# Optimization experiments

Hardware: AMD Instinct MI355X
Metric: run time of the kernel (lower is better)

## Reference

```python
import jax, jax.numpy as jnp
import numpy as np
from jax import lax

NUM_POINT = 2048   # S: number of FPS-sampled centers
RADIUS = 0.2       # ball-query radius
NUM_SAMPLE = 32    # K: neighbors per center


def setup_inputs() -> dict:
    key = jax.random.key(0)
    k1, k2 = jax.random.split(key)
    B, N, C = 4, 8192, 64
    xyz = jax.random.normal(k1, (B, N, 3), dtype=jnp.float32)
    features = jax.random.normal(k2, (B, C, N), dtype=jnp.float32)
    return {"xyz": xyz, "features": features}


def fps(xyz, npoint):
    """D-FPS (farthest point sampling on coords). xyz (B,N,3) -> idx (B,npoint) int32.
    Matches CUDA FPS: start at index 0, iteratively pick argmax of min-dist."""
    B, N, _ = xyz.shape

    def body(carry, _):
        min_d, last = carry
        p = jnp.take_along_axis(xyz, last[:, None, None], axis=1)  # (B,1,3)
        d = jnp.sum((xyz - p) ** 2, axis=-1)                        # (B,N)
        min_d = jnp.minimum(min_d, d)
        nxt = jnp.argmax(min_d, axis=-1).astype(jnp.int32)
        return (min_d, nxt), nxt

    idx0 = jnp.zeros((B,), jnp.int32)
    min_d0 = jnp.full((B, N), 1e10, dtype=xyz.dtype)
    (_, _), rest = lax.scan(body, (min_d0, idx0), None, length=npoint - 1)
    return jnp.concatenate([idx0[None], rest], axis=0).T  # (B, npoint)


def ball_query(radius, nsample, xyz, new_xyz):
    """For each center pick the first nsample point indices (in original order)
    with squared dist < radius^2; pad short lists with the first hit (0 if none).
    xyz (B,N,3), new_xyz (B,S,3) -> idx (B,S,nsample) int32."""
    N = xyz.shape[1]
    d2 = jnp.sum((new_xyz[:, :, None, :] - xyz[:, None, :, :]) ** 2, axis=-1)  # (B,S,N)
    mask = d2 < radius * radius
    # key = point index where in-ball, else N; nsample smallest keys = first hits in order
    key = jnp.where(mask, jnp.arange(N, dtype=jnp.int32)[None, None, :], N)
    _, idx = lax.top_k(-key, nsample)            # (B,S,nsample)
    idx = idx.astype(jnp.int32)
    valid = jnp.take_along_axis(mask, idx, axis=-1)
    first = jnp.where(valid[:, :, :1], idx[:, :, :1], 0)
    return jnp.where(valid, idx, first)


def reference(xyz, features):
    B, N, _ = xyz.shape
    C = features.shape[1]
    fps_idx = fps(xyz, NUM_POINT)                                       # (B,S)
    new_xyz = jnp.take_along_axis(xyz, fps_idx[:, :, None], axis=1)     # (B,S,3)
    idx = ball_query(RADIUS, NUM_SAMPLE, xyz, new_xyz)                  # (B,S,K)
    # grouped xyz, recentered on each sampled point
    grouped_xyz = jnp.take_along_axis(xyz[:, None], idx[..., None], axis=2)  # (B,S,K,3)
    grouped_xyz = grouped_xyz - new_xyz[:, :, None, :]
    # grouped features
    f = jnp.swapaxes(features, 1, 2)                                    # (B,N,C)
    grouped_f = jnp.take_along_axis(f[:, None], idx[..., None], axis=2)  # (B,S,K,C)
    # use_xyz=True: concat relative coords with features -> (B, 3+C, S, K)
    grouped = jnp.concatenate([grouped_xyz, grouped_f], axis=-1).transpose(0, 3, 1, 2)
    return (new_xyz, grouped, fps_idx)
```

## Files before the change

kernel.cpp:

```cpp
#include <hip/hip_runtime.h>

#define NPTS 8192
#define SPTS 2048
#define KS 32
#define CF 64
#define BQ 4
#define FPS_T 512
#define PPT (NPTS / FPS_T)
#define PPT2 (PPT / 2)
#define FPS_SHIFT 9

#define OFF_GROUPED 24576
#define GROUPED_SZ  17563648
#define OFF_FPSIDX  (OFF_GROUPED + GROUPED_SZ)

typedef __attribute__((ext_vector_type(2))) float vf2;
typedef unsigned long long u64;

#define DPPMAXF(x, ctrl) do {                                                   \
    int _t = __builtin_amdgcn_mov_dpp(__float_as_int(x), (ctrl), 0xf, 0xf, true); \
    x = fmaxf((x), __int_as_float(_t));                                         \
} while (0)

#define DPPMAXU(x, ctrl) do {                                                   \
    unsigned _u = (unsigned)__builtin_amdgcn_mov_dpp((int)(x), (ctrl), 0xf, 0xf, true); \
    x = ((x) > _u) ? (x) : _u;                                                  \
} while (0)

__global__ __launch_bounds__(FPS_T)
void fps_kernel(const float* __restrict__ xyz, float* __restrict__ out)
{
#pragma clang fp contract(off)
    __shared__ float sx[NPTS], sy[NPTS], sz[NPTS];
    __shared__ u64 slots[2][8];
    const int b    = blockIdx.x;
    const int tid  = threadIdx.x;
    const int wv   = tid >> 6;
    const int lane = tid & 63;
    const float* xb = xyz + (size_t)b * (NPTS * 3);

    vf2 PX[PPT2], PY[PPT2], PZ[PPT2], MD[PPT2];
#pragma unroll
    for (int j = 0; j < PPT2; ++j) {
        const int p0 = tid + FPS_T * (2 * j);
        const int p1 = p0 + FPS_T;
        const float x0 = xb[p0 * 3 + 0], y0 = xb[p0 * 3 + 1], z0 = xb[p0 * 3 + 2];
        const float x1 = xb[p1 * 3 + 0], y1 = xb[p1 * 3 + 1], z1 = xb[p1 * 3 + 2];
        sx[p0] = x0; sy[p0] = y0; sz[p0] = z0;
        sx[p1] = x1; sy[p1] = y1; sz[p1] = z1;
        vf2 vx; vx.x = x0; vx.y = x1; PX[j] = vx;
        vf2 vy; vy.x = y0; vy.y = y1; PY[j] = vy;
        vf2 vz; vz.x = z0; vz.y = z1; PZ[j] = vz;
        vf2 vm; vm.x = 1e10f; vm.y = 1e10f; MD[j] = vm;
    }

    float* newxyz = out;
    float* fpsidx = out + OFF_FPSIDX;

    float qx = xb[0], qy = xb[1], qz = xb[2];
    if (tid == 0) {
        fpsidx[(size_t)b * SPTS + 0] = 0.0f;
        newxyz[(size_t)b * SPTS * 3 + 0] = qx;
        newxyz[(size_t)b * SPTS * 3 + 1] = qy;
        newxyz[(size_t)b * SPTS * 3 + 2] = qz;
    }

    for (int i = 1; i < SPTS; ++i) {
        vf2 qxx; qxx.x = qx; qxx.y = qx;
        vf2 qyy; qyy.x = qy; qyy.y = qy;
        vf2 qzz; qzz.x = qz; qzz.y = qz;

#pragma unroll
        for (int j = 0; j < PPT2; ++j) {
            const vf2 dx = PX[j] - qxx;
            const vf2 dy = PY[j] - qyy;
            const vf2 dz = PZ[j] - qzz;
            const vf2 d  = (dx * dx + dy * dy) + dz * dz;
            MD[j] = __builtin_elementwise_min(MD[j], d);
        }

        vf2 m0 = __builtin_elementwise_max(MD[0], MD[1]);
        vf2 m1 = __builtin_elementwise_max(MD[2], MD[3]);
        vf2 m2 = __builtin_elementwise_max(MD[4], MD[5]);
        vf2 m3 = __builtin_elementwise_max(MD[6], MD[7]);
        m0 = __builtin_elementwise_max(m0, m1);
        m2 = __builtin_elementwise_max(m2, m3);
        m0 = __builtin_elementwise_max(m0, m2);
        const float best = fmaxf(m0.x, m0.y);

        int bj = PPT - 1;
#pragma unroll
        for (int j = PPT - 2; j >= 0; --j) {
            const float v = (j & 1) ? MD[j >> 1].y : MD[j >> 1].x;
            if (v == best) bj = j;
        }
        const int bidx = tid + (bj << FPS_SHIFT);

        float wm = best;
        DPPMAXF(wm, 0x111);
        DPPMAXF(wm, 0x112);
        DPPMAXF(wm, 0x114);
        DPPMAXF(wm, 0x118);
        DPPMAXF(wm, 0x142);
        DPPMAXF(wm, 0x143);
        const float wavemax =
            __int_as_float(__builtin_amdgcn_readlane(__float_as_int(wm), 63));

        unsigned cand = (best == wavemax) ? (unsigned)(NPTS - 1 - bidx) : 0u;
        DPPMAXU(cand, 0x111);
        DPPMAXU(cand, 0x112);
        DPPMAXU(cand, 0x114);
        DPPMAXU(cand, 0x118);
        DPPMAXU(cand, 0x142);
        DPPMAXU(cand, 0x143);
        const unsigned candmax =
            (unsigned)__builtin_amdgcn_readlane((int)cand, 63);

        const u64 pk = ((u64)__float_as_uint(wavemax) << 32) | candmax;
        if (lane == 0) slots[i & 1][wv] = pk;
        __syncthreads();

        u64 g = slots[i & 1][0];
#pragma unroll
        for (int w = 1; w < 8; ++w) {
            const u64 s = slots[i & 1][w];
            if (s > g) g = s;
        }
        const int widx = (NPTS - 1) - (int)(unsigned)(g & 0xffffffffull);

        qx = sx[widx]; qy = sy[widx]; qz = sz[widx];

        if (tid == 0) {
            fpsidx[(size_t)b * SPTS + i] = (float)widx;
            const size_t o = ((size_t)b * SPTS + i) * 3;
            newxyz[o + 0] = qx; newxyz[o + 1] = qy; newxyz[o + 2] = qz;
        }
    }
}

__global__ __launch_bounds__(256)
void ballgroup_kernel(const float* __restrict__ xyz, const float* __restrict__ feat,
                      float* out)
{
#pragma clang fp contract(off)
    __shared__ int idxl[4][KS];
    const int tid    = threadIdx.x;
    const int wv     = tid >> 6;
    const int lane   = tid & 63;
    const int center = blockIdx.x * 4 + wv;
    const int b      = center >> 11;
    const int s      = center & (SPTS - 1);
    const float* xb  = xyz + (size_t)b * (NPTS * 3);
    const float* newxyz = out;
    const float cx = newxyz[(size_t)center * 3 + 0];
    const float cy = newxyz[(size_t)center * 3 + 1];
    const float cz = newxyz[(size_t)center * 3 + 2];

    if (lane == 0) idxl[wv][0] = 0;

    int cnt = 0;
    for (int nb = 0; nb < NPTS; nb += 64) {
        const int p = nb + lane;
        const float x = xb[p * 3 + 0];
        const float y = xb[p * 3 + 1];
        const float z = xb[p * 3 + 2];
        const float dx = cx - x, dy = cy - y, dz = cz - z;
        const float d2 = (dx * dx + dy * dy) + dz * dz;
        const bool in = (d2 <= 0.04f);
        const unsigned long long mk = __ballot(in);
        if (in) {
            const int pos = cnt + __popcll(mk & ((1ull << lane) - 1ull));
            if (pos < KS) idxl[wv][pos] = p;
        }
        cnt += (int)__popcll(mk);
        if (cnt >= KS) break;
    }
    const int cc = cnt < KS ? cnt : KS;

    int myidx = 0;
    if (lane < KS) {
        myidx = (lane < cc) ? idxl[wv][lane] : idxl[wv][0];
        idxl[wv][lane] = myidx;
    }

    float* grouped = out + OFF_GROUPED;
    const size_t chstride = (size_t)SPTS * KS;
    const size_t base67   = (size_t)b * 67 * chstride + (size_t)s * KS;

    if (lane < KS) {
        const float gx = xb[(size_t)myidx * 3 + 0] - cx;
        const float gy = xb[(size_t)myidx * 3 + 1] - cy;
        const float gz = xb[(size_t)myidx * 3 + 2] - cz;
        grouped[base67 + 0 * chstride + lane] = gx;
        grouped[base67 + 1 * chstride + lane] = gy;
        grouped[base67 + 2 * chstride + lane] = gz;
    }

    const int k    = lane & (KS - 1);
    const int half = lane >> 5;
    const int gi   = idxl[wv][k];
    const float* fb = feat + (size_t)b * CF * NPTS;
    const size_t obase = base67 + 3 * chstride + (size_t)k;
#pragma unroll 8
    for (int c0 = 0; c0 < 32; ++c0) {
        const int c = c0 * 2 + half;
        grouped[obase + (size_t)c * chstride] = fb[(size_t)c * NPTS + gi];
    }
}

extern "C" void kernel_launch(void* const* d_in, const int* in_sizes, int n_in,
                              void* d_out, int out_size, void* d_ws, size_t ws_size,
                              hipStream_t stream) {
    const float* xyz  = (const float*)d_in[0];
    const float* feat = (const float*)d_in[1];
    float* out = (float*)d_out;
    fps_kernel<<<dim3(BQ), dim3(FPS_T), 0, stream>>>(xyz, out);
    ballgroup_kernel<<<dim3((BQ * SPTS) / 4), dim3(256), 0, stream>>>(xyz, feat, out);
}
```

Measured before the change: 1.907 ms.

## Assign contiguous points per thread in FPS to replace index DPP reduction with ballot

Each FPS thread now owns a contiguous run of 16 points instead of points strided by the block size. Lower lanes then always hold lower indices, so the argmax tie-break can use a ballot plus count-trailing-zeros to find the first lane holding the wave max. That replaces the second six-step DPP max reduction over candidate indices. The per-thread first-match search becomes a bitmask plus ctz. The cost is strided, uncoalesced global loads and possible LDS bank conflicts in the one-time setup, in exchange for a shorter serial reduction in each of the 2047 iterations.

```diff
diff --git a/kernel.cpp b/kernel.cpp
--- a/kernel.cpp
+++ b/kernel.cpp
@@ -6,9 +6,8 @@
 #define CF 64
 #define BQ 4
 #define FPS_T 512
-#define PPT (NPTS / FPS_T)
+#define PPT 16
 #define PPT2 (PPT / 2)
-#define FPS_SHIFT 9
 
 #define OFF_GROUPED 24576
 #define GROUPED_SZ  17563648
@@ -20,11 +19,6 @@
 #define DPPMAXF(x, ctrl) do {                                                   \
     int _t = __builtin_amdgcn_mov_dpp(__float_as_int(x), (ctrl), 0xf, 0xf, true); \
     x = fmaxf((x), __int_as_float(_t));                                         \
-} while (0)
-
-#define DPPMAXU(x, ctrl) do {                                                   \
-    unsigned _u = (unsigned)__builtin_amdgcn_mov_dpp((int)(x), (ctrl), 0xf, 0xf, true); \
-    x = ((x) > _u) ? (x) : _u;                                                  \
 } while (0)
 
 __global__ __launch_bounds__(FPS_T)
@@ -42,8 +36,8 @@
     vf2 PX[PPT2], PY[PPT2], PZ[PPT2], MD[PPT2];
 #pragma unroll
     for (int j = 0; j < PPT2; ++j) {
-        const int p0 = tid + FPS_T * (2 * j);
-        const int p1 = p0 + FPS_T;
+        const int p0 = tid * PPT + 2 * j;
+        const int p1 = p0 + 1;
         const float x0 = xb[p0 * 3 + 0], y0 = xb[p0 * 3 + 1], z0 = xb[p0 * 3 + 2];
         const float x1 = xb[p1 * 3 + 0], y1 = xb[p1 * 3 + 1], z1 = xb[p1 * 3 + 2];
         sx[p0] = x0; sy[p0] = y0; sz[p0] = z0;
@@ -87,14 +81,6 @@
         m2 = __builtin_elementwise_max(m2, m3);
         m0 = __builtin_elementwise_max(m0, m2);
         const float best = fmaxf(m0.x, m0.y);
-
-        int bj = PPT - 1;
-#pragma unroll
-        for (int j = PPT - 2; j >= 0; --j) {
-            const float v = (j & 1) ? MD[j >> 1].y : MD[j >> 1].x;
-            if (v == best) bj = j;
-        }
-        const int bidx = tid + (bj << FPS_SHIFT);
 
         float wm = best;
         DPPMAXF(wm, 0x111);
@@ -106,18 +92,21 @@
         const float wavemax =
             __int_as_float(__builtin_amdgcn_readlane(__float_as_int(wm), 63));
 
-        unsigned cand = (best == wavemax) ? (unsigned)(NPTS - 1 - bidx) : 0u;
-        DPPMAXU(cand, 0x111);
-        DPPMAXU(cand, 0x112);
-        DPPMAXU(cand, 0x114);
-        DPPMAXU(cand, 0x118);
-        DPPMAXU(cand, 0x142);
-        DPPMAXU(cand, 0x143);
-        const unsigned candmax =
-            (unsigned)__builtin_amdgcn_readlane((int)cand, 63);
-
-        const u64 pk = ((u64)__float_as_uint(wavemax) << 32) | candmax;
-        if (lane == 0) slots[i & 1][wv] = pk;
+        unsigned m = 0u;
+#pragma unroll
+        for (int j = 0; j < PPT2; ++j) {
+            m |= (MD[j].x == best) ? (1u << (2 * j))     : 0u;
+            m |= (MD[j].y == best) ? (1u << (2 * j + 1)) : 0u;
+        }
+        const int bo = __builtin_ctz(m);
+
+        const u64 tied = __ballot(best == wavemax);
+        const int fl   = (int)__builtin_ctzll(tied);
+        if (lane == fl) {
+            const unsigned widx_w = (unsigned)(tid * PPT + bo);
+            slots[i & 1][wv] =
+                ((u64)__float_as_uint(wavemax) << 32) | (unsigned)(NPTS - 1 - widx_w);
+        }
         __syncthreads();
 
         u64 g = slots[i & 1][0];
```

After: 2.109 ms. 1.11x slower.
